# Performance work log

Hardware: AMD Instinct MI355X
Metric: run time of the kernel (lower is better)

Reference implementation:

```python
import jax, jax.numpy as jnp
import numpy as np

N = 16        # state dim n
M = 8         # control dim m
T = 50        # time_steps
DT = 0.01     # delta_t
SQRT_DT = DT ** 0.5
GAMMA = 0.1
SIGMA = 0.2
TAU = 0.5
H = 10        # hidden width of subnets
BATCH = 32768


def _mlp(params, x):
    W1, b1, W2, b2, W3, b3 = params
    h = jnp.tanh(x @ W1 + b1)
    h = jnp.tanh(h @ W2 + b2)
    return h @ W3 + b3


def setup_inputs() -> dict:
    key = jax.random.key(0)
    ks = jax.random.split(key, 32)

    def dense(k, i, o):
        return (jax.random.normal(k, (i, o), jnp.float32) / np.float32(np.sqrt(i)))

    inp = {
        'dw': jax.random.normal(ks[0], (T, BATCH, 1), jnp.float32) * SQRT_DT,
        'X0': jax.random.uniform(ks[1], (BATCH, N), jnp.float32),
        'A': dense(ks[2], N, N),
        'Bmat': dense(ks[3], N, M),
        'Cmat': dense(ks[4], N, N),
        'Dmat': dense(ks[5], N, M),
        # phi: (n+1) -> 10 -> 10 -> m
        'phi_W1': dense(ks[6], N + 1, H), 'phi_b1': jnp.zeros((H,), jnp.float32),
        'phi_W2': dense(ks[7], H, H),     'phi_b2': jnp.zeros((H,), jnp.float32),
        'phi_W3': dense(ks[8], H, M),     'phi_b3': jnp.zeros((M,), jnp.float32),
        # Z: (n+1) -> 10 -> 10 -> n
        'Z_W1': dense(ks[9], N + 1, H),   'Z_b1': jnp.zeros((H,), jnp.float32),
        'Z_W2': dense(ks[10], H, H),      'Z_b2': jnp.zeros((H,), jnp.float32),
        'Z_W3': dense(ks[11], H, N),      'Z_b3': jnp.zeros((N,), jnp.float32),
        # Y0: n -> 10 -> 10 -> n
        'Y0_W1': dense(ks[12], N, H),     'Y0_b1': jnp.zeros((H,), jnp.float32),
        'Y0_W2': dense(ks[13], H, H),     'Y0_b2': jnp.zeros((H,), jnp.float32),
        'Y0_W3': dense(ks[14], H, N),     'Y0_b3': jnp.zeros((N,), jnp.float32),
    }
    return inp


def reference(dw, X0, A, Bmat, Cmat, Dmat,
              phi_W1, phi_b1, phi_W2, phi_b2, phi_W3, phi_b3,
              Z_W1, Z_b1, Z_W2, Z_b2, Z_W3, Z_b3,
              Y0_W1, Y0_b1, Y0_W2, Y0_b2, Y0_W3, Y0_b3):
    phi_p = (phi_W1, phi_b1, phi_W2, phi_b2, phi_W3, phi_b3)
    Z_p = (Z_W1, Z_b1, Z_W2, Z_b2, Z_W3, Z_b3)
    Y0_p = (Y0_W1, Y0_b1, Y0_W2, Y0_b2, Y0_W3, Y0_b3)

    B = X0.shape[0]
    Y = _mlp(Y0_p, X0)                              # [B, n]
    t_grid = jnp.arange(T, dtype=X0.dtype) * DT     # [T]
    w_trap = jnp.ones((T,), X0.dtype).at[1:-1].set(2.0)  # trapezoid weights

    def step(carry, xs):
        X, Yc, lc = carry
        dwi, t, w = xs                              # dwi: [B,1]
        state = jnp.concatenate(
            [jnp.broadcast_to(t, (B, 1)).astype(X.dtype), X], axis=1)  # [B, n+1]
        Zv = _mlp(Z_p, state)                       # [B, n]
        u = _mlp(phi_p, state)                      # [B, m] (project = identity)
        # b_mult(M, x) == x @ M.T
        drift_X = X @ A.T + u @ Bmat.T + GAMMA      # [B, n]
        diffusion_X = X @ Cmat.T + u @ Dmat.T + SIGMA
        drift_Y = -(Yc @ A + Zv @ Cmat + X)         # f_x(X,u) = X
        # stop_recording branch: gradient of dH / pre_phi
        dH = Yc @ Bmat + Zv @ Dmat + u              # f_u(X,u) = u -> [B, m]
        pre_phi = jax.lax.stop_gradient(u - TAU * dH)
        Xn = X + drift_X * DT + dwi * diffusion_X
        Yn = Yc + drift_Y * DT + dwi * Zv
        lc = lc + 0.5 * DT * w * jnp.sum(jnp.square(u - pre_phi), axis=1)
        return (Xn, Yn, lc), None

    init = (X0, Y, jnp.zeros((B,), X0.dtype))
    (X, Y, loss_control), _ = jax.lax.scan(step, init, (dw, t_grid, w_trap))
    loss_bsde = jnp.sum(jnp.square(Y - X), axis=1)  # g_x(X) = X
    return jnp.stack([jnp.mean(loss_bsde), jnp.mean(loss_control)])
```

## Files before the change

### kernel.cpp

```cpp
#include <hip/hip_runtime.h>

namespace {

typedef float v4f __attribute__((ext_vector_type(4)));
typedef _Float16 half4 __attribute__((ext_vector_type(4)));
typedef __fp16 fp16x2 __attribute__((ext_vector_type(2)));

constexpr int   kB     = 32768;
constexpr int   kT     = 50;
constexpr float kDT    = 0.01f;
constexpr float kGamma = 0.1f;
constexpr float kSigma = 0.2f;
constexpr float kTau   = 0.5f;
constexpr float kA     = 2.8853900817779268f;


__device__ __forceinline__ float fexp2(float x) {
#if __has_builtin(__builtin_amdgcn_exp2f)
  return __builtin_amdgcn_exp2f(x);
#else
  return exp2f(x);
#endif
}

__device__ __forceinline__ float fact(float x) {
  return __builtin_amdgcn_rcpf(fexp2(x) + 1.0f);
}

__device__ __forceinline__ v4f act4(v4f a) {
  v4f r;
  r[0] = fact(a[0]); r[1] = fact(a[1]);
  r[2] = fact(a[2]); r[3] = fact(a[3]);
  return r;
}

__global__ __launch_bounds__(64)
__attribute__((amdgpu_waves_per_eu(2, 2)))
void bsde_kernel(const float* __restrict__ dw, const float* __restrict__ X0,
                 const float* __restrict__ A,   const float* __restrict__ Bm,
                 const float* __restrict__ Cm,  const float* __restrict__ Dm,
                 const float* __restrict__ pW1, const float* __restrict__ pb1,
                 const float* __restrict__ pW2, const float* __restrict__ pb2,
                 const float* __restrict__ pW3, const float* __restrict__ pb3,
                 const float* __restrict__ zW1, const float* __restrict__ zb1,
                 const float* __restrict__ zW2, const float* __restrict__ zb2,
                 const float* __restrict__ zW3, const float* __restrict__ zb3,
                 const float* __restrict__ yW1, const float* __restrict__ yb1,
                 const float* __restrict__ yW2, const float* __restrict__ yb2,
                 const float* __restrict__ yW3, const float* __restrict__ yb3,
                 float* __restrict__ out)
{
  const int lane = threadIdx.x;
  const int col  = lane & 15;
  const int quad = lane >> 4;
  const int e    = blockIdx.x * 16 + col;
  const int bq   = quad * 4;
  const int m    = col;

  auto wv = [&](int p, int k) -> float {
    switch (p) {
      case 0:  return (m < 10) ? kA * yW1[k * 10 + m] : 0.f;
      case 1:  return (m < 10 && k < 10) ? -2.f * kA * yW2[k * 10 + m] : 0.f;
      case 2:  return (k < 10) ? -2.f * yW3[k * 16 + m] : 0.f;
      case 3:  return (m < 10) ? kA * zW1[(k + 1) * 10 + m] : 0.f;
      case 4:  return (m < 10) ? kA * pW1[(k + 1) * 10 + m] : 0.f;
      case 5:  return (m < 10 && k < 10) ? -2.f * kA * zW2[k * 10 + m] : 0.f;
      case 6:  return (m < 10 && k < 10) ? -2.f * kA * pW2[k * 10 + m] : 0.f;
      case 7:  return (k < 10) ? -2.f * zW3[k * 16 + m] : 0.f;
      case 8:  return (m < 8 && k < 10) ? -2.f * pW3[k * 8 + m] : 0.f;
      case 9:  return A[m * 16 + k];
      case 10: return (k < 8) ? Bm[m * 8 + k] : 0.f;
      case 11: return Cm[m * 16 + k];
      case 12: return (k < 8) ? Dm[m * 8 + k] : 0.f;
      case 13: return A[k * 16 + m];
      case 14: return Cm[k * 16 + m];
      case 15: return (m < 8) ? Bm[k * 8 + m] : 0.f;
      case 16: return (m < 8) ? Dm[k * 8 + m] : 0.f;
    }
    return 0.f;
  };

  half4 af[17];
#pragma unroll
  for (int p = 0; p < 17; ++p) {
#pragma unroll
    for (int j = 0; j < 4; ++j) af[p][j] = (_Float16)wv(p, 4 * quad + j);
  }

  auto sum10 = [](const float* W, int stride, int mm) {
    float s = 0.f;
#pragma unroll
    for (int j = 0; j < 10; ++j) s += W[j * stride + mm];
    return s;
  };

  v4f cy1, cy2, cy3, c2z, c2p, c3z, c3p, vtz, vbz, vtp, vbp;
#pragma unroll
  for (int r = 0; r < 4; ++r) {
    const int mm = bq + r;
    const bool m10 = mm < 10, m8 = mm < 8;
    cy1[r] = m10 ? kA * yb1[mm] : 0.f;
    cy2[r] = m10 ? kA * (yb2[mm] + sum10(yW2, 10, mm)) : 0.f;
    cy3[r] = yb3[mm] + sum10(yW3, 16, mm);
    c2z[r] = m10 ? kA * (zb2[mm] + sum10(zW2, 10, mm)) : 0.f;
    c2p[r] = m10 ? kA * (pb2[mm] + sum10(pW2, 10, mm)) : 0.f;
    c3z[r] = zb3[mm] + sum10(zW3, 16, mm);
    c3p[r] = m8 ? (pb3[mm] + sum10(pW3, 8, mm)) : 0.f;
    vtz[r] = m10 ? kA * zW1[mm] : 0.f;
    vbz[r] = m10 ? kA * zb1[mm] : 0.f;
    vtp[r] = m10 ? kA * pW1[mm] : 0.f;
    vbp[r] = m10 ? kA * pb1[mm] : 0.f;
  }

  auto pk4 = [](v4f a) -> half4 {
#if __has_builtin(__builtin_amdgcn_cvt_pkrtz)
    union { fp16x2 p[2]; half4 h; } z;
    z.p[0] = __builtin_amdgcn_cvt_pkrtz(a[0], a[1]);
    z.p[1] = __builtin_amdgcn_cvt_pkrtz(a[2], a[3]);
    return z.h;
#else
    half4 h;
    h[0] = (_Float16)a[0]; h[1] = (_Float16)a[1];
    h[2] = (_Float16)a[2]; h[3] = (_Float16)a[3];
    return h;
#endif
  };
  auto mm4 = [](half4 a, half4 b, v4f c) -> v4f {
    return __builtin_amdgcn_mfma_f32_16x16x16f16(a, b, c, 0, 0, 0);
  };

  const v4f gam4  = {kGamma, kGamma, kGamma, kGamma};
  const v4f sig4  = {kSigma, kSigma, kSigma, kSigma};
  const v4f zero4 = {0.f, 0.f, 0.f, 0.f};

  v4f x4 = *(const v4f*)&X0[e * 16 + bq];
  half4 xB = pk4(x4);
  v4f y4;
  {
    v4f h = mm4(af[0], xB, cy1);
    v4f g = mm4(af[1], pk4(act4(h)), cy2);
    y4    = mm4(af[2], pk4(act4(g)), cy3);
  }

  float lcp = 0.0f;
  float dwv = dw[e];

#pragma unroll 1
  for (int t = 0; t < kT; ++t) {
    float dwn = (t < kT - 1) ? dw[(t + 1) * kB + e] : 0.0f;
    const float tv = (float)t * kDT;
    const float wt = (t == 0 || t == kT - 1) ? 1.0f : 2.0f;

    half4 yB = pk4(y4);

    v4f dx1 = mm4(af[9],  xB, gam4);
    v4f fx1 = mm4(af[11], xB, sig4);
    v4f dy1 = mm4(af[13], yB, x4);
    v4f dh1 = mm4(af[15], yB, zero4);

    v4f c1z, c1p;
#pragma unroll
    for (int r = 0; r < 4; ++r) {
      c1z[r] = vbz[r] + tv * vtz[r];
      c1p[r] = vbp[r] + tv * vtp[r];
    }

    v4f hz = mm4(af[3], xB, c1z);
    v4f hp = mm4(af[4], xB, c1p);
    v4f gz = mm4(af[5], pk4(act4(hz)), c2z);
    v4f gp = mm4(af[6], pk4(act4(hp)), c2p);
    v4f zv = mm4(af[7], pk4(act4(gz)), c3z);
    v4f uu = mm4(af[8], pk4(act4(gp)), c3p);

    half4 zB = pk4(zv);
    half4 uB = pk4(uu);
    v4f dx = mm4(af[10], uB, dx1);
    v4f fx = mm4(af[12], uB, fx1);
    v4f dy = mm4(af[14], zB, dy1);
    v4f dh = mm4(af[16], zB, dh1);

    float ss = 0.0f;
    v4f Xn, Yn;
#pragma unroll
    for (int r = 0; r < 4; ++r) {
      Xn[r] = x4[r] + kDT * dx[r] + dwv * fx[r];
      Yn[r] = y4[r] - kDT * dy[r] + dwv * zv[r];
      float d = dh[r] + uu[r];
      ss += d * d;
    }
    lcp += (0.5f * kDT * kTau * kTau) * wt * ss;
    x4 = Xn; y4 = Yn;
    xB = pk4(x4);
    dwv = dwn;
  }

  float bp = 0.0f;
#pragma unroll
  for (int r = 0; r < 4; ++r) { float d = y4[r] - x4[r]; bp += d * d; }

#pragma unroll
  for (int s = 32; s > 0; s >>= 1) {
    bp  += __shfl_down(bp,  s, 64);
    lcp += __shfl_down(lcp, s, 64);
  }
  if (lane == 0) {
    atomicAdd(&out[0], bp  * (1.0f / (float)kB));
    atomicAdd(&out[1], lcp * (1.0f / (float)kB));
  }
}

}

extern "C" void kernel_launch(void* const* d_in, const int* in_sizes, int n_in,
                              void* d_out, int out_size, void* d_ws, size_t ws_size,
                              hipStream_t stream) {
  (void)in_sizes; (void)n_in; (void)ws_size; (void)out_size; (void)d_ws;

  const float* dw  = (const float*)d_in[0];
  const float* X0  = (const float*)d_in[1];
  const float* A   = (const float*)d_in[2];
  const float* Bm  = (const float*)d_in[3];
  const float* Cm  = (const float*)d_in[4];
  const float* Dm  = (const float*)d_in[5];
  const float* pW1 = (const float*)d_in[6];
  const float* pb1 = (const float*)d_in[7];
  const float* pW2 = (const float*)d_in[8];
  const float* pb2 = (const float*)d_in[9];
  const float* pW3 = (const float*)d_in[10];
  const float* pb3 = (const float*)d_in[11];
  const float* zW1 = (const float*)d_in[12];
  const float* zb1 = (const float*)d_in[13];
  const float* zW2 = (const float*)d_in[14];
  const float* zb2 = (const float*)d_in[15];
  const float* zW3 = (const float*)d_in[16];
  const float* zb3 = (const float*)d_in[17];
  const float* yW1 = (const float*)d_in[18];
  const float* yb1 = (const float*)d_in[19];
  const float* yW2 = (const float*)d_in[20];
  const float* yb2 = (const float*)d_in[21];
  const float* yW3 = (const float*)d_in[22];
  const float* yb3 = (const float*)d_in[23];
  float* out = (float*)d_out;

  (void)hipMemsetAsync(out, 0, 2 * sizeof(float), stream);

  bsde_kernel<<<kB / 16, 64, 0, stream>>>(
      dw, X0, A, Bm, Cm, Dm,
      pW1, pb1, pW2, pb2, pW3, pb3,
      zW1, zb1, zW2, zb2, zW3, zb3,
      yW1, yb1, yW2, yb2, yW3, yb3, out);
}
```

Before: 191.5 us.

## Precompute fused weight fragments and compute next-step first-layer preactivations algebraically

Adds a prep kernel that packs all MFMA weight fragments and bias vectors into the workspace, including products of the first-layer Z/phi weights with A, B, C, D. The main kernel loads these instead of rebuilding them per block. The next step's first-layer preactivations are computed directly from the current X, u and dw through the composed matrices, which takes the hz/hp MFMAs off the serial critical path after Xn. The cost is extra MFMAs per step, more fragment registers, an extra launch, and some fp16 rounding differences from the precomposed weights.

```diff
diff --git a/kernel.cpp b/kernel.cpp
--- a/kernel.cpp
+++ b/kernel.cpp
@@ -5,6 +5,7 @@
 typedef float v4f __attribute__((ext_vector_type(4)));
 typedef _Float16 half4 __attribute__((ext_vector_type(4)));
 typedef __fp16 fp16x2 __attribute__((ext_vector_type(2)));
+typedef unsigned int uint32;
 
 constexpr int   kB     = 32768;
 constexpr int   kT     = 50;
@@ -14,6 +15,9 @@
 constexpr float kTau   = 0.5f;
 constexpr float kA     = 2.8853900817779268f;
 
+constexpr int kNFrag      = 25;
+constexpr int kFragDwords = kNFrag * 128;
+constexpr int kBiasFloats = 13 * 16;
 
 __device__ __forceinline__ float fexp2(float x) {
 #if __has_builtin(__builtin_amdgcn_exp2f)
@@ -34,96 +38,152 @@
   return r;
 }
 
+__device__ __forceinline__ uint32 pk2rtn(float a, float b) {
+  union { _Float16 h[2]; uint32 u; } z;
+  z.h[0] = (_Float16)a; z.h[1] = (_Float16)b;
+  return z.u;
+}
+
+__global__ __launch_bounds__(64) void prep_kernel(
+    const float* __restrict__ A,   const float* __restrict__ Bm,
+    const float* __restrict__ Cm,  const float* __restrict__ Dm,
+    const float* __restrict__ pW1, const float* __restrict__ pb1,
+    const float* __restrict__ pW2, const float* __restrict__ pb2,
+    const float* __restrict__ pW3, const float* __restrict__ pb3,
+    const float* __restrict__ zW1, const float* __restrict__ zb1,
+    const float* __restrict__ zW2, const float* __restrict__ zb2,
+    const float* __restrict__ zW3, const float* __restrict__ zb3,
+    const float* __restrict__ yW1, const float* __restrict__ yb1,
+    const float* __restrict__ yW2, const float* __restrict__ yb2,
+    const float* __restrict__ yW3, const float* __restrict__ yb3,
+    uint32* __restrict__ ws)
+{
+  const int tid = threadIdx.x;
+  const int blk = blockIdx.x;
+
+  auto sum10 = [](const float* W, int stride, int mm) {
+    float s = 0.f;
+#pragma unroll
+    for (int j = 0; j < 10; ++j) s += W[j * stride + mm];
+    return s;
+  };
+
+  if (blk < kNFrag) {
+    const int m = tid & 15, q = tid >> 4;
+    const int p = blk;
+
+    auto comp = [&](const float* W1, const float* M, int ncol, int k,
+                    float scale) -> float {
+      if (m >= 10 || k >= ncol) return 0.f;
+      float s = 0.f;
+#pragma unroll
+      for (int i = 0; i < 16; ++i) s += W1[(i + 1) * 10 + m] * M[i * ncol + k];
+      return kA * scale * s;
+    };
+
+    auto wv = [&](int k) -> float {
+      switch (p) {
+        case 0:  return (m < 10) ? kA * yW1[k * 10 + m] : 0.f;
+        case 1:  return (m < 10 && k < 10) ? -2.f * kA * yW2[k * 10 + m] : 0.f;
+        case 2:  return (k < 10) ? -2.f * yW3[k * 16 + m] : 0.f;
+        case 3:  return (m < 10) ? kA * zW1[(k + 1) * 10 + m] : 0.f;
+        case 4:  return (m < 10) ? kA * pW1[(k + 1) * 10 + m] : 0.f;
+        case 5:  return (m < 10 && k < 10) ? -2.f * kA * zW2[k * 10 + m] : 0.f;
+        case 6:  return (m < 10 && k < 10) ? -2.f * kA * pW2[k * 10 + m] : 0.f;
+        case 7:  return (k < 10) ? -2.f * zW3[k * 16 + m] : 0.f;
+        case 8:  return (m < 8 && k < 10) ? -2.f * pW3[k * 8 + m] : 0.f;
+        case 9:  return A[m * 16 + k];
+        case 10: return (k < 8) ? Bm[m * 8 + k] : 0.f;
+        case 11: return Cm[m * 16 + k];
+        case 12: return (k < 8) ? Dm[m * 8 + k] : 0.f;
+        case 13: return A[k * 16 + m];
+        case 14: return Cm[k * 16 + m];
+        case 15: return (m < 8) ? Bm[k * 8 + m] : 0.f;
+        case 16: return (m < 8) ? Dm[k * 8 + m] : 0.f;
+        case 17: return comp(zW1, A,  16, k, kDT);
+        case 18: return comp(zW1, Cm, 16, k, 1.f);
+        case 19: return comp(zW1, Bm,  8, k, kDT);
+        case 20: return comp(zW1, Dm,  8, k, 1.f);
+        case 21: return comp(pW1, A,  16, k, kDT);
+        case 22: return comp(pW1, Cm, 16, k, 1.f);
+        case 23: return comp(pW1, Bm,  8, k, kDT);
+        case 24: return comp(pW1, Dm,  8, k, 1.f);
+      }
+      return 0.f;
+    };
+
+    const int k0 = 4 * q;
+    ws[p * 128 + tid * 2]     = pk2rtn(wv(k0),     wv(k0 + 1));
+    ws[p * 128 + tid * 2 + 1] = pk2rtn(wv(k0 + 2), wv(k0 + 3));
+  } else {
+    float* bsf = (float*)(ws + kFragDwords);
+    auto sumx = [&](const float* W1, int mm) {
+      float s = 0.f;
+#pragma unroll
+      for (int i = 0; i < 16; ++i) s += W1[(i + 1) * 10 + mm];
+      return kA * s;
+    };
+    auto bval = [&](int a, int mm) -> float {
+      const bool m10 = mm < 10;
+      switch (a) {
+        case 0:  return m10 ? kA * yb1[mm] : 0.f;
+        case 1:  return m10 ? kA * (yb2[mm] + sum10(yW2, 10, mm)) : 0.f;
+        case 2:  return yb3[mm] + sum10(yW3, 16, mm);
+        case 3:  return m10 ? kA * (zb2[mm] + sum10(zW2, 10, mm)) : 0.f;
+        case 4:  return m10 ? kA * (pb2[mm] + sum10(pW2, 10, mm)) : 0.f;
+        case 5:  return zb3[mm] + sum10(zW3, 16, mm);
+        case 6:  return (mm < 8) ? pb3[mm] + sum10(pW3, 8, mm) : 0.f;
+        case 7:  return m10 ? kA * zW1[mm] : 0.f;
+        case 8:  return m10 ? kA * zb1[mm] : 0.f;
+        case 9:  return m10 ? kA * pW1[mm] : 0.f;
+        case 10: return m10 ? kA * pb1[mm] : 0.f;
+        case 11: return m10 ? sumx(zW1, mm) : 0.f;
+        case 12: return m10 ? sumx(pW1, mm) : 0.f;
+      }
+      return 0.f;
+    };
+    for (int j = tid; j < kBiasFloats; j += 64) {
+      bsf[j] = bval(j >> 4, j & 15);
+    }
+  }
+}
+
 __global__ __launch_bounds__(64)
 __attribute__((amdgpu_waves_per_eu(2, 2)))
 void bsde_kernel(const float* __restrict__ dw, const float* __restrict__ X0,
-                 const float* __restrict__ A,   const float* __restrict__ Bm,
-                 const float* __restrict__ Cm,  const float* __restrict__ Dm,
-                 const float* __restrict__ pW1, const float* __restrict__ pb1,
-                 const float* __restrict__ pW2, const float* __restrict__ pb2,
-                 const float* __restrict__ pW3, const float* __restrict__ pb3,
-                 const float* __restrict__ zW1, const float* __restrict__ zb1,
-                 const float* __restrict__ zW2, const float* __restrict__ zb2,
-                 const float* __restrict__ zW3, const float* __restrict__ zb3,
-                 const float* __restrict__ yW1, const float* __restrict__ yb1,
-                 const float* __restrict__ yW2, const float* __restrict__ yb2,
-                 const float* __restrict__ yW3, const float* __restrict__ yb3,
-                 float* __restrict__ out)
+                 const uint32* __restrict__ wsu, float* __restrict__ out)
 {
   const int lane = threadIdx.x;
   const int col  = lane & 15;
   const int quad = lane >> 4;
   const int e    = blockIdx.x * 16 + col;
   const int bq   = quad * 4;
-  const int m    = col;
-
-  auto wv = [&](int p, int k) -> float {
-    switch (p) {
-      case 0:  return (m < 10) ? kA * yW1[k * 10 + m] : 0.f;
-      case 1:  return (m < 10 && k < 10) ? -2.f * kA * yW2[k * 10 + m] : 0.f;
-      case 2:  return (k < 10) ? -2.f * yW3[k * 16 + m] : 0.f;
-      case 3:  return (m < 10) ? kA * zW1[(k + 1) * 10 + m] : 0.f;
-      case 4:  return (m < 10) ? kA * pW1[(k + 1) * 10 + m] : 0.f;
-      case 5:  return (m < 10 && k < 10) ? -2.f * kA * zW2[k * 10 + m] : 0.f;
-      case 6:  return (m < 10 && k < 10) ? -2.f * kA * pW2[k * 10 + m] : 0.f;
-      case 7:  return (k < 10) ? -2.f * zW3[k * 16 + m] : 0.f;
-      case 8:  return (m < 8 && k < 10) ? -2.f * pW3[k * 8 + m] : 0.f;
-      case 9:  return A[m * 16 + k];
-      case 10: return (k < 8) ? Bm[m * 8 + k] : 0.f;
-      case 11: return Cm[m * 16 + k];
-      case 12: return (k < 8) ? Dm[m * 8 + k] : 0.f;
-      case 13: return A[k * 16 + m];
-      case 14: return Cm[k * 16 + m];
-      case 15: return (m < 8) ? Bm[k * 8 + m] : 0.f;
-      case 16: return (m < 8) ? Dm[k * 8 + m] : 0.f;
-    }
-    return 0.f;
-  };
-
-  half4 af[17];
-#pragma unroll
-  for (int p = 0; p < 17; ++p) {
-#pragma unroll
-    for (int j = 0; j < 4; ++j) af[p][j] = (_Float16)wv(p, 4 * quad + j);
-  }
-
-  auto sum10 = [](const float* W, int stride, int mm) {
-    float s = 0.f;
-#pragma unroll
-    for (int j = 0; j < 10; ++j) s += W[j * stride + mm];
-    return s;
-  };
-
-  v4f cy1, cy2, cy3, c2z, c2p, c3z, c3p, vtz, vbz, vtp, vbp;
-#pragma unroll
-  for (int r = 0; r < 4; ++r) {
-    const int mm = bq + r;
-    const bool m10 = mm < 10, m8 = mm < 8;
-    cy1[r] = m10 ? kA * yb1[mm] : 0.f;
-    cy2[r] = m10 ? kA * (yb2[mm] + sum10(yW2, 10, mm)) : 0.f;
-    cy3[r] = yb3[mm] + sum10(yW3, 16, mm);
-    c2z[r] = m10 ? kA * (zb2[mm] + sum10(zW2, 10, mm)) : 0.f;
-    c2p[r] = m10 ? kA * (pb2[mm] + sum10(pW2, 10, mm)) : 0.f;
-    c3z[r] = zb3[mm] + sum10(zW3, 16, mm);
-    c3p[r] = m8 ? (pb3[mm] + sum10(pW3, 8, mm)) : 0.f;
-    vtz[r] = m10 ? kA * zW1[mm] : 0.f;
-    vbz[r] = m10 ? kA * zb1[mm] : 0.f;
-    vtp[r] = m10 ? kA * pW1[mm] : 0.f;
-    vbp[r] = m10 ? kA * pb1[mm] : 0.f;
-  }
+
+  half4 af[kNFrag];
+#pragma unroll
+  for (int p = 0; p < kNFrag; ++p) {
+    union { uint2 u; half4 h; } z;
+    z.u = *(const uint2*)(wsu + p * 128 + lane * 2);
+    af[p] = z.h;
+  }
+
+  const float* bsf = (const float*)(wsu + kFragDwords);
+  const v4f c2z  = *(const v4f*)&bsf[3 * 16 + bq];
+  const v4f c2p  = *(const v4f*)&bsf[4 * 16 + bq];
+  const v4f c3z  = *(const v4f*)&bsf[5 * 16 + bq];
+  const v4f c3p  = *(const v4f*)&bsf[6 * 16 + bq];
+  const v4f vtz  = *(const v4f*)&bsf[7 * 16 + bq];
+  const v4f vbz  = *(const v4f*)&bsf[8 * 16 + bq];
+  const v4f vtp  = *(const v4f*)&bsf[9 * 16 + bq];
+  const v4f vbp  = *(const v4f*)&bsf[10 * 16 + bq];
+  const v4f w1sz = *(const v4f*)&bsf[11 * 16 + bq];
+  const v4f w1sp = *(const v4f*)&bsf[12 * 16 + bq];
 
   auto pk4 = [](v4f a) -> half4 {
-#if __has_builtin(__builtin_amdgcn_cvt_pkrtz)
     union { fp16x2 p[2]; half4 h; } z;
     z.p[0] = __builtin_amdgcn_cvt_pkrtz(a[0], a[1]);
     z.p[1] = __builtin_amdgcn_cvt_pkrtz(a[2], a[3]);
     return z.h;
-#else
-    half4 h;
-    h[0] = (_Float16)a[0]; h[1] = (_Float16)a[1];
-    h[2] = (_Float16)a[2]; h[3] = (_Float16)a[3];
-    return h;
-#endif
   };
   auto mm4 = [](half4 a, half4 b, v4f c) -> v4f {
     return __builtin_amdgcn_mfma_f32_16x16x16f16(a, b, c, 0, 0, 0);
@@ -137,19 +197,29 @@
   half4 xB = pk4(x4);
   v4f y4;
   {
+    const v4f cy1 = *(const v4f*)&bsf[0 * 16 + bq];
+    const v4f cy2 = *(const v4f*)&bsf[1 * 16 + bq];
+    const v4f cy3 = *(const v4f*)&bsf[2 * 16 + bq];
     v4f h = mm4(af[0], xB, cy1);
     v4f g = mm4(af[1], pk4(act4(h)), cy2);
     y4    = mm4(af[2], pk4(act4(g)), cy3);
   }
+  v4f hzp = mm4(af[3], xB, vbz);
+  v4f hpp = mm4(af[4], xB, vbp);
+
+  float dwv = dw[e];
+  v4f xs0;
+#pragma unroll
+  for (int r = 0; r < 4; ++r) xs0[r] = x4[r] * dwv;
+  half4 xDB = pk4(xs0);
 
   float lcp = 0.0f;
-  float dwv = dw[e];
 
 #pragma unroll 1
   for (int t = 0; t < kT; ++t) {
-    float dwn = (t < kT - 1) ? dw[(t + 1) * kB + e] : 0.0f;
-    const float tv = (float)t * kDT;
-    const float wt = (t == 0 || t == kT - 1) ? 1.0f : 2.0f;
+    const float dwn = (t < kT - 1) ? dw[(t + 1) * kB + e] : 0.0f;
+    const float tvn = (float)(t + 1) * kDT;
+    const float wt  = (t == 0 || t == kT - 1) ? 1.0f : 2.0f;
 
     half4 yB = pk4(y4);
 
@@ -158,26 +228,38 @@
     v4f dy1 = mm4(af[13], yB, x4);
     v4f dh1 = mm4(af[15], yB, zero4);
 
-    v4f c1z, c1p;
+    const float gs = kDT * kGamma + dwv * kSigma;
+    v4f Cz, Cp;
 #pragma unroll
     for (int r = 0; r < 4; ++r) {
-      c1z[r] = vbz[r] + tv * vtz[r];
-      c1p[r] = vbp[r] + tv * vtp[r];
+      Cz[r] = vbz[r] + tvn * vtz[r] + gs * w1sz[r];
+      Cp[r] = vbp[r] + tvn * vtp[r] + gs * w1sp[r];
     }
-
-    v4f hz = mm4(af[3], xB, c1z);
-    v4f hp = mm4(af[4], xB, c1p);
-    v4f gz = mm4(af[5], pk4(act4(hz)), c2z);
-    v4f gp = mm4(af[6], pk4(act4(hp)), c2p);
+    v4f Ez = mm4(af[18], xDB, mm4(af[17], xB, mm4(af[3], xB, Cz)));
+    v4f Ep = mm4(af[22], xDB, mm4(af[21], xB, mm4(af[4], xB, Cp)));
+
+    v4f gz = mm4(af[5], pk4(act4(hzp)), c2z);
+    v4f gp = mm4(af[6], pk4(act4(hpp)), c2p);
     v4f zv = mm4(af[7], pk4(act4(gz)), c3z);
     v4f uu = mm4(af[8], pk4(act4(gp)), c3p);
 
     half4 zB = pk4(zv);
     half4 uB = pk4(uu);
-    v4f dx = mm4(af[10], uB, dx1);
-    v4f fx = mm4(af[12], uB, fx1);
-    v4f dy = mm4(af[14], zB, dy1);
-    v4f dh = mm4(af[16], zB, dh1);
+
+    v4f dx  = mm4(af[10], uB, dx1);
+    v4f fx  = mm4(af[12], uB, fx1);
+    v4f dy  = mm4(af[14], zB, dy1);
+    v4f dh  = mm4(af[16], zB, dh1);
+    v4f l1z = mm4(af[19], uB, Ez);
+    v4f l2z = mm4(af[20], uB, zero4);
+    v4f l1p = mm4(af[23], uB, Ep);
+    v4f l2p = mm4(af[24], uB, zero4);
+
+#pragma unroll
+    for (int r = 0; r < 4; ++r) {
+      hzp[r] = l1z[r] + dwv * l2z[r];
+      hpp[r] = l1p[r] + dwv * l2p[r];
+    }
 
     float ss = 0.0f;
     v4f Xn, Yn;
@@ -191,6 +273,10 @@
     lcp += (0.5f * kDT * kTau * kTau) * wt * ss;
     x4 = Xn; y4 = Yn;
     xB = pk4(x4);
+    v4f xs;
+#pragma unroll
+    for (int r = 0; r < 4; ++r) xs[r] = x4[r] * dwn;
+    xDB = pk4(xs);
     dwv = dwn;
   }
 
@@ -214,7 +300,7 @@
 extern "C" void kernel_launch(void* const* d_in, const int* in_sizes, int n_in,
                               void* d_out, int out_size, void* d_ws, size_t ws_size,
                               hipStream_t stream) {
-  (void)in_sizes; (void)n_in; (void)ws_size; (void)out_size; (void)d_ws;
+  (void)in_sizes; (void)n_in; (void)ws_size; (void)out_size;
 
   const float* dw  = (const float*)d_in[0];
   const float* X0  = (const float*)d_in[1];
@@ -241,12 +327,15 @@
   const float* yW3 = (const float*)d_in[22];
   const float* yb3 = (const float*)d_in[23];
   float* out = (float*)d_out;
+  unsigned int* ws = (unsigned int*)d_ws;
 
   (void)hipMemsetAsync(out, 0, 2 * sizeof(float), stream);
 
-  bsde_kernel<<<kB / 16, 64, 0, stream>>>(
-      dw, X0, A, Bm, Cm, Dm,
+  prep_kernel<<<26, 64, 0, stream>>>(
+      A, Bm, Cm, Dm,
       pW1, pb1, pW2, pb2, pW3, pb3,
       zW1, zb1, zW2, zb2, zW3, zb3,
-      yW1, yb1, yW2, yb2, yW3, yb3, out);
-}
+      yW1, yb1, yW2, yb2, yW3, yb3, ws);
+
+  bsde_kernel<<<kB / 16, 64, 0, stream>>>(dw, X0, ws, out);
+}
```

Measured after the change: 199.4 us. +4.2%, slower.
